# Kernel tuning notes

Measured on AMD Instinct MI355X. Metric: run time of the kernel, lower is better.

The kernel has to match this reference:

```python
import math
import jax, jax.numpy as jnp
import numpy as np

B, D, E, R, TOP_K = 16384, 2048, 64, 128, 2
TAU = 1.0
CAP_FACTOR = 1.25
TOP_C = min(E, max(4, 2 * TOP_K))  # GatingNetwork default top_c


def setup_inputs() -> dict:
    key = jax.random.key(0)
    ks = jax.random.split(key, 7)
    x = jax.random.normal(ks[0], (B, D), dtype=jnp.float32)
    # shared_encoder: nn.Linear(d, d) -> weight [out, in], bias [out]
    We = jax.random.normal(ks[1], (D, D), dtype=jnp.float32) / np.sqrt(D)
    be = jnp.zeros((D,), dtype=jnp.float32)
    # gating: nn.Linear(d, E, bias=False) -> weight [E, d]
    Wg = jax.random.normal(ks[2], (E, D), dtype=jnp.float32) / np.sqrt(D)
    # LowRankExpert per expert: U [r, d], V [d, r], gamma scalar (init 1.0)
    U = jax.random.normal(ks[3], (E, R, D), dtype=jnp.float32) / np.sqrt(D)
    V = jax.random.normal(ks[4], (E, D, R), dtype=jnp.float32) / np.sqrt(R)
    gamma = jnp.ones((E,), dtype=jnp.float32)
    return {"x": x, "We": We, "be": be, "Wg": Wg, "U": U, "V": V, "gamma": gamma}


def reference(x, We, be, Wg, U, V, gamma):
    # shared encoder
    enc = x @ We.T + be  # [B, D]

    # ---- gating: top-C candidates then top-K routing ----
    logits = (enc @ Wg.T) / TAU  # [B, E]
    topc_vals, topc_idx = jax.lax.top_k(logits, TOP_C)          # [B, C]
    topk_vals, pos_in_c = jax.lax.top_k(topc_vals, TOP_K)       # [B, K]
    topk_idx = jnp.take_along_axis(topc_idx, pos_in_c, axis=1)  # [B, K]
    # masked stable softmax over the K selected logits (with 1e-12 eps as in source)
    m = jnp.max(topk_vals, axis=-1, keepdims=True)
    ex = jnp.exp(topk_vals - m)
    w = ex / (jnp.sum(ex, axis=-1, keepdims=True) + 1e-12)      # [B, K]

    # ---- flatten assignments ----
    N = B * TOP_K
    tok = jnp.repeat(jnp.arange(B), TOP_K)   # [N]
    eid = topk_idx.reshape(-1)               # [N]
    wf = w.reshape(-1)                       # [N]
    wmask = wf > 1e-12

    # ---- capacity-based dispatch (sort/group equivalent, fixed shapes) ----
    cap = int(math.ceil(CAP_FACTOR * N / E))  # expert capacity
    onehot = ((eid[:, None] == jnp.arange(E)[None, :]) & wmask[:, None]).astype(jnp.int32)  # [N, E]
    pos = jnp.cumsum(onehot, axis=0) - onehot                      # position within expert
    pos_of = jnp.take_along_axis(pos, eid[:, None], axis=1)[:, 0]  # [N]
    valid = wmask & (pos_of < cap)
    slot = jnp.where(valid, pos_of, cap)  # overflow -> dummy slot (never occurs at this cap)

    # gather tokens to per-expert buffers [E, cap+1, D]
    xbuf = jnp.zeros((E, cap + 1, D), dtype=enc.dtype).at[eid, slot].set(enc[tok])

    # batched low-rank experts: delta = gamma * V @ silu(U @ x)
    h = jax.nn.silu(jnp.einsum('ecd,erd->ecr', xbuf, U))
    delta = jnp.einsum('ecr,edr->ecd', h, V) * gamma[:, None, None]  # [E, cap+1, D]

    # scatter-combine: y = enc + sum_k w_k * delta_k (residual handled since sum w = 1)
    dflat = delta[eid, slot]  # [N, D]
    y = enc.at[tok].add(jnp.where(valid, wf, 0.0)[:, None] * dflat)
    return y
```

## Files before the change

### kernel.cpp

```cpp
#include <hip/hip_runtime.h>
#include <math.h>

#define NTOK 16384
#define DDIM 2048
#define NEXP 64
#define RRANK 128
#define CAP 640

typedef __attribute__((ext_vector_type(8))) short bf16x8;
typedef __attribute__((ext_vector_type(4))) float f32x4;
typedef __attribute__((address_space(1))) const unsigned int gu32_t;
typedef __attribute__((address_space(3))) unsigned int lu32_t;

__device__ __forceinline__ void gload16(const void* g, void* l) {
  __builtin_amdgcn_global_load_lds((gu32_t*)g, (lu32_t*)l, 16, 0, 0);
}

__device__ __forceinline__ float silu_f(float v) {
  return v / (1.f + expf(-v));
}

__device__ __forceinline__ unsigned short f2bf(float f) {
  unsigned int u = __float_as_uint(f);
  unsigned int r = (u + 0x7fffu + ((u >> 16) & 1u)) >> 16;
  return (unsigned short)r;
}

__device__ __forceinline__ float bf2f(unsigned short u) {
  return __uint_as_float(((unsigned int)u) << 16);
}

__device__ __forceinline__ int swz256(int d) {
  return d ^ (((d >> 8) & 7) << 4);
}

__global__ __launch_bounds__(256) void cvt_all_kernel(
    const float* __restrict__ x, const float* __restrict__ We,
    const float* __restrict__ U, const float* __restrict__ V,
    unsigned short* __restrict__ xb, unsigned short* __restrict__ Web,
    unsigned short* __restrict__ Ub, unsigned short* __restrict__ Vb)
{
  const int S0 = NTOK * DDIM / 4;
  const int S1 = DDIM * DDIM / 4;
  const int S2 = NEXP * RRANK * DDIM / 4;
  const int total = S0 + S1 + 2 * S2;
  int i = blockIdx.x * 256 + threadIdx.x;
  const int stride = gridDim.x * 256;
  for (; i < total; i += stride) {
    const float* in; unsigned short* out; int j;
    if (i < S0) { in = x; out = xb; j = i; }
    else if (i < S0 + S1) { in = We; out = Web; j = i - S0; }
    else if (i < S0 + S1 + S2) { in = U; out = Ub; j = i - S0 - S1; }
    else { in = V; out = Vb; j = i - S0 - S1 - S2; }
    const float4 v = ((const float4*)in)[j];
    ushort4 o;
    o.x = f2bf(v.x); o.y = f2bf(v.y); o.z = f2bf(v.z); o.w = f2bf(v.w);
    ((ushort4*)out)[j] = o;
  }
}

__global__ __launch_bounds__(256) void enc_mfma4(
    const unsigned short* __restrict__ xb, const unsigned short* __restrict__ Web,
    const float* __restrict__ be, unsigned short* __restrict__ encbf)
{
  __shared__ unsigned short At[128 * 64];
  __shared__ unsigned short Bt[128 * 64];
  const int tid = threadIdx.x;
  const int lane = tid & 63, wid = tid >> 6;
  const int wr = wid >> 1, wc = wid & 1;
  const int fr = lane & 15, fq = lane >> 4;
  const int bid = blockIdx.x;
  const int wg = (bid & 7) * 256 + (bid >> 3);
  const int n0 = (wg & 15) * 128, m0 = (wg >> 4) * 128;

  const unsigned short* asrc[4];
  const unsigned short* bsrc[4];
  char* adst[4];
  char* bdst[4];
#pragma unroll
  for (int is = 0; is < 4; ++is) {
    const int doff = is * 4096 + tid * 16;
    const int r = doff >> 7;
    const int cs = ((doff >> 4) & 7) ^ (r & 7);
    asrc[is] = xb + (size_t)(m0 + r) * DDIM + cs * 8;
    bsrc[is] = Web + (size_t)(n0 + r) * DDIM + cs * 8;
    adst[is] = (char*)At + doff;
    bdst[is] = (char*)Bt + doff;
  }

  f32x4 acc[4][4];
#pragma unroll
  for (int m = 0; m < 4; ++m)
#pragma unroll
    for (int n = 0; n < 4; ++n) acc[m][n] = (f32x4){0.f, 0.f, 0.f, 0.f};

  for (int kb = 0; kb < DDIM; kb += 64) {
    __syncthreads();
#pragma unroll
    for (int is = 0; is < 4; ++is) {
      gload16(asrc[is] + kb, adst[is]);
      gload16(bsrc[is] + kb, bdst[is]);
    }
    __syncthreads();
#pragma unroll
    for (int kk = 0; kk < 2; ++kk) {
      bf16x8 af[4], bfv[4];
#pragma unroll
      for (int m = 0; m < 4; ++m) {
        const int row = wr * 64 + m * 16 + fr;
        af[m] = *(const bf16x8*)((const char*)At +
                 row * 128 + (((kk * 4 + fq) ^ (row & 7)) << 4));
      }
#pragma unroll
      for (int n = 0; n < 4; ++n) {
        const int row = wc * 64 + n * 16 + fr;
        bfv[n] = *(const bf16x8*)((const char*)Bt +
                  row * 128 + (((kk * 4 + fq) ^ (row & 7)) << 4));
      }
#pragma unroll
      for (int m = 0; m < 4; ++m)
#pragma unroll
        for (int n = 0; n < 4; ++n)
          acc[m][n] = __builtin_amdgcn_mfma_f32_16x16x32_bf16(af[m], bfv[n], acc[m][n], 0, 0, 0);
    }
  }

  float bias[4];
#pragma unroll
  for (int n = 0; n < 4; ++n) bias[n] = be[n0 + wc * 64 + n * 16 + fr];
#pragma unroll
  for (int m = 0; m < 4; ++m) {
#pragma unroll
    for (int j = 0; j < 4; ++j) {
      const int row = m0 + wr * 64 + m * 16 + fq * 4 + j;
      unsigned short* ob = encbf + (size_t)row * DDIM + n0 + wc * 64 + fr;
#pragma unroll
      for (int n = 0; n < 4; ++n)
        ob[n * 16] = f2bf(acc[m][n][j] + bias[n]);
    }
  }
}

__global__ __launch_bounds__(256) void gmat_part_kernel(
    const float* __restrict__ We, const float* __restrict__ Wg,
    double* __restrict__ Gpart)
{
  __shared__ float As[64][68];
  __shared__ float Bs[64][68];
  const int tid = threadIdx.x;
  const int d0 = blockIdx.x * 64;
  const int oc = blockIdx.y;
  const int tx = tid & 15, ty = tid >> 4;
  const int row = tid >> 2, p = (tid & 3) * 16;

  double acc[4][4];
#pragma unroll
  for (int j = 0; j < 4; ++j)
#pragma unroll
    for (int i = 0; i < 4; ++i) acc[j][i] = 0.0;

  for (int o0 = oc * 256; o0 < oc * 256 + 256; o0 += 64) {
    float4 wv[4], gv[4];
#pragma unroll
    for (int q = 0; q < 4; ++q) {
      wv[q] = *(const float4*)(We + (size_t)(o0 + row) * DDIM + d0 + p + q * 4);
      gv[q] = *(const float4*)(Wg + (size_t)row * DDIM + o0 + p + q * 4);
    }
    __syncthreads();
#pragma unroll
    for (int q = 0; q < 4; ++q) {
      const int c = p + q * 4;
      As[row][c + 0] = wv[q].x; As[row][c + 1] = wv[q].y;
      As[row][c + 2] = wv[q].z; As[row][c + 3] = wv[q].w;
      Bs[c + 0][row] = gv[q].x; Bs[c + 1][row] = gv[q].y;
      Bs[c + 2][row] = gv[q].z; Bs[c + 3][row] = gv[q].w;
    }
    __syncthreads();
#pragma unroll 8
    for (int oo = 0; oo < 64; ++oo) {
      double a[4], b[4];
#pragma unroll
      for (int j = 0; j < 4; ++j) a[j] = (double)As[oo][ty * 4 + j];
#pragma unroll
      for (int i = 0; i < 4; ++i) b[i] = (double)Bs[oo][tx * 4 + i];
#pragma unroll
      for (int j = 0; j < 4; ++j)
#pragma unroll
        for (int i = 0; i < 4; ++i)
          acc[j][i] = fma(a[j], b[i], acc[j][i]);
    }
    __syncthreads();
  }
#pragma unroll
  for (int j = 0; j < 4; ++j)
#pragma unroll
    for (int i = 0; i < 4; ++i) {
      const int d = d0 + ty * 4 + j, e = tx * 4 + i;
      Gpart[(size_t)oc * (DDIM * NEXP) + (size_t)e * DDIM + d] = acc[j][i];
    }
}

__global__ __launch_bounds__(256) void greduce_kernel(
    const double* __restrict__ Gpart, double* __restrict__ Gt,
    unsigned short* __restrict__ Gbf)
{
  const int idx = blockIdx.x * 256 + threadIdx.x;
  double s = 0.0;
#pragma unroll
  for (int oc = 0; oc < 8; ++oc)
    s += Gpart[(size_t)oc * (DDIM * NEXP) + idx];
  Gt[idx] = s;
  Gbf[idx] = f2bf((float)s);
}

__global__ __launch_bounds__(256) void bias_c_kernel(
    const float* __restrict__ be, const float* __restrict__ Wg,
    double* __restrict__ c64)
{
  const int e = blockIdx.x;
  const int tid = threadIdx.x;
  double s = 0.0;
  for (int o = tid; o < DDIM; o += 256)
    s += (double)be[o] * (double)Wg[(size_t)e * DDIM + o];
  __shared__ double red[256];
  red[tid] = s;
  __syncthreads();
  for (int st = 128; st > 0; st >>= 1) {
    if (tid < st) red[tid] += red[tid + st];
    __syncthreads();
  }
  if (tid == 0) c64[e] = red[0];
}

__global__ __launch_bounds__(256) void logits_topc_kernel(
    const unsigned short* __restrict__ xb, const unsigned short* __restrict__ Gbf,
    const double* __restrict__ c64, int* __restrict__ cand8)
{
  __shared__ unsigned short At[128 * 32];
  __shared__ unsigned short Bt[64 * 32];
  __shared__ float Ls[128][64];
  const int tid = threadIdx.x;
  const int lane = tid & 63, wid = tid >> 6;
  const int fr = lane & 15, fq = lane >> 4;
  const int t0 = blockIdx.x * 128;

  const int doff0 = wid * 1024 + lane * 16;
  const int doff1 = doff0 + 4096;
  const unsigned short* as0 = xb + (size_t)(t0 + (doff0 >> 6)) * DDIM + ((doff0 & 63) >> 1);
  const unsigned short* as1 = xb + (size_t)(t0 + (doff1 >> 6)) * DDIM + ((doff1 & 63) >> 1);
  const unsigned short* bs0 = Gbf + (size_t)(doff0 >> 6) * DDIM + ((doff0 & 63) >> 1);
  char* ad0 = (char*)At + doff0; char* ad1 = (char*)At + doff1;
  char* bd0 = (char*)Bt + doff0;

  f32x4 acc[2][4];
#pragma unroll
  for (int m = 0; m < 2; ++m)
#pragma unroll
    for (int n = 0; n < 4; ++n) acc[m][n] = (f32x4){0.f, 0.f, 0.f, 0.f};

  for (int kb = 0; kb < DDIM; kb += 32) {
    __syncthreads();
    gload16(as0 + kb, ad0);
    gload16(as1 + kb, ad1);
    gload16(bs0 + kb, bd0);
    __syncthreads();
    bf16x8 af[2], bfr[4];
#pragma unroll
    for (int m = 0; m < 2; ++m)
      af[m] = *(const bf16x8*)&At[(wid * 32 + m * 16 + fr) * 32 + fq * 8];
#pragma unroll
    for (int n = 0; n < 4; ++n)
      bfr[n] = *(const bf16x8*)&Bt[(n * 16 + fr) * 32 + fq * 8];
#pragma unroll
    for (int m = 0; m < 2; ++m)
#pragma unroll
      for (int n = 0; n < 4; ++n)
        acc[m][n] = __builtin_amdgcn_mfma_f32_16x16x32_bf16(af[m], bfr[n], acc[m][n], 0, 0, 0);
  }

#pragma unroll
  for (int m = 0; m < 2; ++m)
#pragma unroll
    for (int j = 0; j < 4; ++j) {
      const int row = wid * 32 + m * 16 + fq * 4 + j;
#pragma unroll
      for (int n = 0; n < 4; ++n)
        Ls[row][n * 16 + fr] = acc[m][n][j];
    }
  __syncthreads();

  if (tid < 128) {
    float v8[8];
    int i8[8];
#pragma unroll
    for (int c = 0; c < 8; ++c) { v8[c] = -INFINITY; i8[c] = 0; }
    for (int e = 0; e < NEXP; ++e) {
      const float v = Ls[tid][e] + (float)c64[e];
      if (v > v8[7]) {
        int p = 7;
        while (p > 0 && v > v8[p - 1]) { v8[p] = v8[p - 1]; i8[p] = i8[p - 1]; --p; }
        v8[p] = v; i8[p] = e;
      }
    }
    int* cp = cand8 + (size_t)(t0 + tid) * 8;
#pragma unroll
    for (int c = 0; c < 8; ++c) cp[c] = i8[c];
  }
}

__global__ __launch_bounds__(256) void refine_kernel(
    const float* __restrict__ x, const double* __restrict__ Gt,
    const double* __restrict__ c64, const int* __restrict__ cand8,
    int* __restrict__ topk, float* __restrict__ wkf)
{
  const int t = blockIdx.x;
  const int tid = threadIdx.x;
  const int lane = tid & 63, w = tid >> 6;
  __shared__ float xs[DDIM];
  __shared__ double red[8][4];

  ((float4*)xs)[tid] = ((const float4*)(x + (size_t)t * DDIM))[tid];
  ((float4*)xs)[tid + 256] = ((const float4*)(x + (size_t)t * DDIM))[tid + 256];
  __syncthreads();

  int myc[8];
#pragma unroll
  for (int c = 0; c < 8; ++c) myc[c] = cand8[(size_t)t * 8 + c];

#pragma unroll
  for (int c = 0; c < 8; ++c) {
    const double* g = Gt + (size_t)myc[c] * DDIM;
    double s = 0.0;
#pragma unroll
    for (int q = 0; q < 8; ++q) {
      const int d = q * 256 + tid;
      s += (double)xs[d] * g[d];
    }
#pragma unroll
    for (int off = 32; off > 0; off >>= 1) s += __shfl_down(s, off);
    if (lane == 0) red[c][w] = s;
  }
  __syncthreads();

  if (tid == 0) {
    double v1 = -1e300, v2 = -1e300;
    int i1 = 0, i2 = 0;
#pragma unroll
    for (int c = 0; c < 8; ++c) {
      const double v = red[c][0] + red[c][1] + red[c][2] + red[c][3] + c64[myc[c]];
      if (v > v1) { v2 = v1; i2 = i1; v1 = v; i1 = myc[c]; }
      else if (v > v2) { v2 = v; i2 = myc[c]; }
    }
    const double e2 = exp(v2 - v1);
    const double s = 1.0 + e2 + 1e-12;
    topk[2 * t] = i1; topk[2 * t + 1] = i2;
    wkf[2 * t] = (float)(1.0 / s);
    wkf[2 * t + 1] = (float)(e2 / s);
  }
}

__global__ __launch_bounds__(256) void route_kernel(
    const int* __restrict__ topk, const float* __restrict__ wkf,
    int* __restrict__ slots , int* __restrict__ counts_eff,
    int* __restrict__ val )
{
  const int e = blockIdx.x;
  const int tid = threadIdx.x;
  const int lane = tid & 63, wave = tid >> 6;
  const int base0 = wave * 8192;
  __shared__ int wcnt[4];

  int cnt = 0;
  for (int c = 0; c < 8192; c += 64) {
    const int a = base0 + c + lane;
    const bool match = (topk[a] == e) && (wkf[a] > 1e-12f);
    cnt += (int)__popcll(__ballot(match));
  }
  if (lane == 0) wcnt[wave] = cnt;
  __syncthreads();

  int run = 0;
  for (int w = 0; w < 4; ++w)
    if (w < wave) run += wcnt[w];
  const int total = wcnt[0] + wcnt[1] + wcnt[2] + wcnt[3];

  for (int c = 0; c < 8192; c += 64) {
    const int a = base0 + c + lane;
    const bool match = (topk[a] == e) && (wkf[a] > 1e-12f);
    const unsigned long long bal = __ballot(match);
    const int rank = run + (int)__popcll(bal & ((1ull << lane) - 1ull));
    if (match && rank < CAP) {
      slots[e * CAP + rank] = a;
      val[a] = 1;
    }
    run += (int)__popcll(bal);
  }
  if (tid == 0) counts_eff[e] = (total < CAP) ? total : CAP;
}

__global__ __launch_bounds__(256) void expert_fused(
    const unsigned short* __restrict__ encbf, const unsigned short* __restrict__ Ub,
    const unsigned short* __restrict__ Vb, const float* __restrict__ gamma,
    const int* __restrict__ counts_eff, const int* __restrict__ slots,
    const float* __restrict__ wkf, unsigned short* __restrict__ Dbuf)
{
  const int lin = blockIdx.x;
  const int wg = (lin & 7) * 80 + (lin >> 3);
  const int e = wg / 10;
  const int t0 = (wg % 10) * 64;
  const int cnt = counts_eff[e];
  if (t0 >= cnt) return;

  __shared__ int aid[64];
  __shared__ int toks[64];
  __shared__ float wts[64];
  __shared__ unsigned short Ht[64 * 128];
  __shared__ char U2[32768];

  const int tid = threadIdx.x;
  const int lane = tid & 63, wid = tid >> 6;
  const int wr = wid >> 1, wc = wid & 1;
  const int fr = lane & 15, fq = lane >> 4;

  if (tid < 64) {
    const int i = t0 + tid;
    if (i < cnt) {
      const int a = slots[e * CAP + i];
      aid[tid] = a;
      toks[tid] = a >> 1;
      wts[tid] = wkf[a] * gamma[e];
    } else {
      aid[tid] = -1;
      toks[tid] = slots[e * CAP] >> 1;
      wts[tid] = 0.f;
    }
  }
  __syncthreads();

  unsigned short* At = (unsigned short*)U2;
  unsigned short* Bt = (unsigned short*)(U2 + 8192);
  const unsigned short* Ue = Ub + (size_t)e * RRANK * DDIM;

  size_t aoff[2]; char* adst[2];
#pragma unroll
  for (int is = 0; is < 2; ++is) {
    const int doff = is * 4096 + tid * 16;
    const int r = doff >> 7;
    const int cs = ((doff >> 4) & 7) ^ (r & 7);
    aoff[is] = (size_t)toks[r] * DDIM + cs * 8;
    adst[is] = (char*)At + doff;
  }
  const unsigned short* bsrc[4]; char* bdst[4];
#pragma unroll
  for (int is = 0; is < 4; ++is) {
    const int doff = is * 4096 + tid * 16;
    const int r = doff >> 7;
    const int cs = ((doff >> 4) & 7) ^ (r & 7);
    bsrc[is] = Ue + (size_t)r * DDIM + cs * 8;
    bdst[is] = (char*)Bt + doff;
  }

  f32x4 hacc[2][4];
#pragma unroll
  for (int m = 0; m < 2; ++m)
#pragma unroll
    for (int n = 0; n < 4; ++n) hacc[m][n] = (f32x4){0.f, 0.f, 0.f, 0.f};

  for (int kb = 0; kb < DDIM; kb += 64) {
    __syncthreads();
    gload16(encbf + aoff[0] + kb, adst[0]);
    gload16(encbf + aoff[1] + kb, adst[1]);
#pragma unroll
    for (int is = 0; is < 4; ++is)
      gload16(bsrc[is] + kb, bdst[is]);
    __syncthreads();
#pragma unroll
    for (int kk = 0; kk < 2; ++kk) {
      bf16x8 af[2], bfv[4];
#pragma unroll
      for (int m = 0; m < 2; ++m) {
        const int row = wr * 32 + m * 16 + fr;
        af[m] = *(const bf16x8*)((const char*)At +
                 row * 128 + (((kk * 4 + fq) ^ (row & 7)) << 4));
      }
#pragma unroll
      for (int n = 0; n < 4; ++n) {
        const int row = wc * 64 + n * 16 + fr;
        bfv[n] = *(const bf16x8*)((const char*)Bt +
                  row * 128 + (((kk * 4 + fq) ^ (row & 7)) << 4));
      }
#pragma unroll
      for (int m = 0; m < 2; ++m)
#pragma unroll
        for (int n = 0; n < 4; ++n)
          hacc[m][n] = __builtin_amdgcn_mfma_f32_16x16x32_bf16(af[m], bfv[n], hacc[m][n], 0, 0, 0);
    }
  }

  __syncthreads();
#pragma unroll
  for (int m = 0; m < 2; ++m) {
#pragma unroll
    for (int j = 0; j < 4; ++j) {
      const int row = wr * 32 + m * 16 + fq * 4 + j;
#pragma unroll
      for (int n = 0; n < 4; ++n) {
        const int col = wc * 64 + n * 16 + fr;
        const int b = (row * 256 + col * 2) ^ ((row & 7) << 4);
        *(unsigned short*)((char*)Ht + b) = f2bf(silu_f(hacc[m][n][j]));
      }
    }
  }
  __syncthreads();

  unsigned short* Vt = (unsigned short*)U2;
  const unsigned short* Ve = Vb + (size_t)e * DDIM * RRANK;
  const int hd = tid * 16;

  bf16x8 paf[2][4];
  float wv[2][4];
  int av[2][4];
#pragma unroll
  for (int m = 0; m < 2; ++m) {
    const int row = wr * 32 + m * 16 + fr;
#pragma unroll
    for (int kk = 0; kk < 4; ++kk) {
      const int b = (row * 256 + kk * 64 + fq * 16) ^ ((row & 7) << 4);
      paf[m][kk] = *(const bf16x8*)((const char*)Ht + b);
    }
#pragma unroll
    for (int j = 0; j < 4; ++j) {
      const int tl = wr * 32 + m * 16 + fq * 4 + j;
      wv[m][j] = wts[tl];
      av[m][j] = aid[tl];
    }
  }

  for (int nb = 0; nb < 16; ++nb) {
    __syncthreads();
    const unsigned short* vsrc = Ve + (size_t)nb * 128 * RRANK;
#pragma unroll
    for (int is = 0; is < 8; ++is) {
      const int d = is * 4096 + hd;
      gload16(vsrc + (swz256(d) >> 1), (char*)Vt + d);
    }
    __syncthreads();

    f32x4 acc[2][4];
#pragma unroll
    for (int m = 0; m < 2; ++m)
#pragma unroll
      for (int n = 0; n < 4; ++n) acc[m][n] = (f32x4){0.f, 0.f, 0.f, 0.f};

#pragma unroll
    for (int n = 0; n < 4; ++n) {
      const int drow = wc * 64 + n * 16 + fr;
#pragma unroll
      for (int kk = 0; kk < 4; ++kk) {
        const int b = (drow * 256 + kk * 64 + fq * 16) ^ ((drow & 7) << 4);
        const bf16x8 bfr = *(const bf16x8*)((const char*)Vt + b);
#pragma unroll
        for (int m = 0; m < 2; ++m)
          acc[m][n] = __builtin_amdgcn_mfma_f32_16x16x32_bf16(paf[m][kk], bfr, acc[m][n], 0, 0, 0);
      }
    }

#pragma unroll
    for (int m = 0; m < 2; ++m) {
#pragma unroll
      for (int j = 0; j < 4; ++j) {
        if (av[m][j] >= 0) {
          const float w = wv[m][j];
          unsigned short* dp = Dbuf + (size_t)av[m][j] * DDIM + nb * 128 + wc * 64 + fr;
#pragma unroll
          for (int n = 0; n < 4; ++n)
            dp[n * 16] = f2bf(acc[m][n][j] * w);
        }
      }
    }
  }
}

__global__ __launch_bounds__(256) void combine_kernel(
    const unsigned short* __restrict__ encbf, const unsigned short* __restrict__ Dbuf,
    const int* __restrict__ val, float* __restrict__ y)
{
  const int t = blockIdx.x;
  const int tid = threadIdx.x;
  const int c0 = tid * 8;
  float* yp = y + (size_t)t * DDIM + c0;
  const int v0 = val[2 * t], v1 = val[2 * t + 1];

  const ushort4 e0 = *(const ushort4*)(encbf + (size_t)t * DDIM + c0);
  const ushort4 e1 = *(const ushort4*)(encbf + (size_t)t * DDIM + c0 + 4);
  float o[8] = {bf2f(e0.x), bf2f(e0.y), bf2f(e0.z), bf2f(e0.w),
                bf2f(e1.x), bf2f(e1.y), bf2f(e1.z), bf2f(e1.w)};

  if (v0) {
    const ushort4 d0 = *(const ushort4*)(Dbuf + (size_t)(2 * t) * DDIM + c0);
    const ushort4 d1 = *(const ushort4*)(Dbuf + (size_t)(2 * t) * DDIM + c0 + 4);
    o[0] += bf2f(d0.x); o[1] += bf2f(d0.y); o[2] += bf2f(d0.z); o[3] += bf2f(d0.w);
    o[4] += bf2f(d1.x); o[5] += bf2f(d1.y); o[6] += bf2f(d1.z); o[7] += bf2f(d1.w);
  }
  if (v1) {
    const ushort4 d0 = *(const ushort4*)(Dbuf + (size_t)(2 * t + 1) * DDIM + c0);
    const ushort4 d1 = *(const ushort4*)(Dbuf + (size_t)(2 * t + 1) * DDIM + c0 + 4);
    o[0] += bf2f(d0.x); o[1] += bf2f(d0.y); o[2] += bf2f(d0.z); o[3] += bf2f(d0.w);
    o[4] += bf2f(d1.x); o[5] += bf2f(d1.y); o[6] += bf2f(d1.z); o[7] += bf2f(d1.w);
  }
  *(float4*)(yp) = (float4){o[0], o[1], o[2], o[3]};
  *(float4*)(yp + 4) = (float4){o[4], o[5], o[6], o[7]};
}

extern "C" void kernel_launch(void* const* d_in, const int* in_sizes, int n_in,
                              void* d_out, int out_size, void* d_ws, size_t ws_size,
                              hipStream_t stream)
{
  const float* x     = (const float*)d_in[0];
  const float* We    = (const float*)d_in[1];
  const float* be    = (const float*)d_in[2];
  const float* Wg    = (const float*)d_in[3];
  const float* U     = (const float*)d_in[4];
  const float* V     = (const float*)d_in[5];
  const float* gamma = (const float*)d_in[6];
  float* y = (float*)d_out;

  char* ws = (char*)d_ws;
  int*            topk       = (int*)(ws + 0);
  float*          wkf        = (float*)(ws + 131072);
  int*            counts_eff = (int*)(ws + 262144);
  double*         c64        = (double*)(ws + 262400);
  int*            cand8      = (int*)(ws + 262912);
  double*         Gt         = (double*)(ws + 787200);
  unsigned short* G_bf       = (unsigned short*)(ws + 1835776);
  int*            slots      = (int*)(ws + 2097920);
  int*            val        = (int*)(ws + 2261760);
  unsigned short* Dbuf       = (unsigned short*)(ws + 2392832);
  unsigned short* x_bf       = (unsigned short*)(ws + 2392832);
  unsigned short* We_bf      = (unsigned short*)(ws + 69501696);
  double*         Gpart      = (double*)(ws + 77890304);
  unsigned short* U_bf       = (unsigned short*)(ws + 136610560);
  unsigned short* V_bf       = (unsigned short*)(ws + 170164992);
  unsigned short* enc_bf     = (unsigned short*)(ws + 203719424);

  hipMemsetAsync(val, 0, 131072, stream);

  cvt_all_kernel<<<dim3(2048), 256, 0, stream>>>(x, We, U, V, x_bf, We_bf, U_bf, V_bf);

  gmat_part_kernel<<<dim3(32, 8), 256, 0, stream>>>(We, Wg, Gpart);
  greduce_kernel<<<dim3(512), 256, 0, stream>>>(Gpart, Gt, G_bf);
  bias_c_kernel<<<dim3(64), 256, 0, stream>>>(be, Wg, c64);
  logits_topc_kernel<<<dim3(128), 256, 0, stream>>>(x_bf, G_bf, c64, cand8);
  refine_kernel<<<dim3(NTOK), 256, 0, stream>>>(x, Gt, c64, cand8, topk, wkf);
  route_kernel<<<dim3(64), 256, 0, stream>>>(topk, wkf, slots, counts_eff, val);

  enc_mfma4<<<dim3(2048), 256, 0, stream>>>(x_bf, We_bf, be, enc_bf);
  expert_fused<<<dim3(640), 256, 0, stream>>>(enc_bf, U_bf, V_bf, gamma, counts_eff, slots, wkf, Dbuf);
  combine_kernel<<<dim3(NTOK), 256, 0, stream>>>(enc_bf, Dbuf, val, y);
}
```

Measured before the change: 731.3 us.

## Double-buffer encoder GEMM with 256x256 tiles and async LDS prefetch

Rewrites the shared encoder bf16 GEMM to use 256x256 block tiles with 512 threads and a double-buffered LDS pipeline. The next k-slab is prefetched via global_load_lds while MFMAs run on the current one, using explicit vmcnt waits and s_setprio around the MFMA bursts. This aims to hide global memory latency and raise data reuse per tile. In exchange it uses 128 KB of LDS and more accumulator registers, which limits occupancy to one block per CU.

```diff
diff --git a/kernel.cpp b/kernel.cpp
--- a/kernel.cpp
+++ b/kernel.cpp
@@ -59,80 +59,110 @@
   }
 }
 
-__global__ __launch_bounds__(256) void enc_mfma4(
+__global__ __launch_bounds__(512, 2) void enc_mfma5(
     const unsigned short* __restrict__ xb, const unsigned short* __restrict__ Web,
     const float* __restrict__ be, unsigned short* __restrict__ encbf)
 {
-  __shared__ unsigned short At[128 * 64];
-  __shared__ unsigned short Bt[128 * 64];
+  __shared__ unsigned short LDS[65536];
   const int tid = threadIdx.x;
   const int lane = tid & 63, wid = tid >> 6;
-  const int wr = wid >> 1, wc = wid & 1;
+  const int wr = wid >> 2, wc = wid & 3;
   const int fr = lane & 15, fq = lane >> 4;
   const int bid = blockIdx.x;
-  const int wg = (bid & 7) * 256 + (bid >> 3);
-  const int n0 = (wg & 15) * 128, m0 = (wg >> 4) * 128;
-
-  const unsigned short* asrc[4];
-  const unsigned short* bsrc[4];
-  char* adst[4];
-  char* bdst[4];
+  const int wg = (bid & 7) * 64 + (bid >> 3);
+  const int n0 = (wg & 7) * 256, m0 = (wg >> 3) * 256;
+
+  const unsigned short* asb[4];
+  const unsigned short* bsb[4];
+  int d4[4];
 #pragma unroll
   for (int is = 0; is < 4; ++is) {
-    const int doff = is * 4096 + tid * 16;
+    const int doff = is * 8192 + tid * 16;
     const int r = doff >> 7;
     const int cs = ((doff >> 4) & 7) ^ (r & 7);
-    asrc[is] = xb + (size_t)(m0 + r) * DDIM + cs * 8;
-    bsrc[is] = Web + (size_t)(n0 + r) * DDIM + cs * 8;
-    adst[is] = (char*)At + doff;
-    bdst[is] = (char*)Bt + doff;
-  }
-
-  f32x4 acc[4][4];
-#pragma unroll
-  for (int m = 0; m < 4; ++m)
+    asb[is] = xb + (size_t)(m0 + r) * DDIM + cs * 8;
+    bsb[is] = Web + (size_t)(n0 + r) * DDIM + cs * 8;
+    d4[is] = doff;
+  }
+
+  auto STAGE = [&](int buf, int kb) {
+#pragma unroll
+    for (int is = 0; is < 4; ++is) {
+      gload16(asb[is] + kb, (char*)(LDS + buf * 16384) + d4[is]);
+      gload16(bsb[is] + kb, (char*)(LDS + 32768 + buf * 16384) + d4[is]);
+    }
+  };
+
+  f32x4 acc[8][4];
+#pragma unroll
+  for (int m = 0; m < 8; ++m)
 #pragma unroll
     for (int n = 0; n < 4; ++n) acc[m][n] = (f32x4){0.f, 0.f, 0.f, 0.f};
 
-  for (int kb = 0; kb < DDIM; kb += 64) {
-    __syncthreads();
-#pragma unroll
-    for (int is = 0; is < 4; ++is) {
-      gload16(asrc[is] + kb, adst[is]);
-      gload16(bsrc[is] + kb, bdst[is]);
-    }
-    __syncthreads();
-#pragma unroll
-    for (int kk = 0; kk < 2; ++kk) {
-      bf16x8 af[4], bfv[4];
+  STAGE(0, 0);
+  STAGE(1, 64);
+  asm volatile("s_waitcnt vmcnt(8)" ::: "memory");
+  __builtin_amdgcn_s_barrier();
+  asm volatile("" ::: "memory");
+
+#pragma unroll 1
+  for (int t = 0; t < 32; ++t) {
+    const int cur = t & 1;
+    const unsigned short* Ab = LDS + cur * 16384;
+    const unsigned short* Bb = LDS + 32768 + cur * 16384;
+
+    bf16x8 bfv[4][2];
+#pragma unroll
+    for (int n = 0; n < 4; ++n) {
+      const int row = wc * 64 + n * 16 + fr;
+#pragma unroll
+      for (int kk = 0; kk < 2; ++kk)
+        bfv[n][kk] = *(const bf16x8*)((const char*)Bb +
+                      row * 128 + (((kk * 4 + fq) ^ (row & 7)) << 4));
+    }
+#pragma unroll
+    for (int mh = 0; mh < 2; ++mh) {
+      bf16x8 af[4][2];
 #pragma unroll
       for (int m = 0; m < 4; ++m) {
-        const int row = wr * 64 + m * 16 + fr;
-        af[m] = *(const bf16x8*)((const char*)At +
-                 row * 128 + (((kk * 4 + fq) ^ (row & 7)) << 4));
+        const int row = wr * 128 + (mh * 4 + m) * 16 + fr;
+#pragma unroll
+        for (int kk = 0; kk < 2; ++kk)
+          af[m][kk] = *(const bf16x8*)((const char*)Ab +
+                       row * 128 + (((kk * 4 + fq) ^ (row & 7)) << 4));
       }
-#pragma unroll
-      for (int n = 0; n < 4; ++n) {
-        const int row = wc * 64 + n * 16 + fr;
-        bfv[n] = *(const bf16x8*)((const char*)Bt +
-                  row * 128 + (((kk * 4 + fq) ^ (row & 7)) << 4));
-      }
+      __builtin_amdgcn_s_setprio(1);
 #pragma unroll
       for (int m = 0; m < 4; ++m)
 #pragma unroll
         for (int n = 0; n < 4; ++n)
-          acc[m][n] = __builtin_amdgcn_mfma_f32_16x16x32_bf16(af[m], bfv[n], acc[m][n], 0, 0, 0);
-    }
+#pragma unroll
+          for (int kk = 0; kk < 2; ++kk)
+            acc[mh * 4 + m][n] = __builtin_amdgcn_mfma_f32_16x16x32_bf16(
+                af[m][kk], bfv[n][kk], acc[mh * 4 + m][n], 0, 0, 0);
+      __builtin_amdgcn_s_setprio(0);
+    }
+
+    asm volatile("" ::: "memory");
+    __builtin_amdgcn_s_barrier();
+    if (t < 30) {
+      STAGE(cur, (t + 2) * 64);
+      asm volatile("s_waitcnt vmcnt(8)" ::: "memory");
+    } else {
+      asm volatile("s_waitcnt vmcnt(0)" ::: "memory");
+    }
+    __builtin_amdgcn_s_barrier();
+    asm volatile("" ::: "memory");
   }
 
   float bias[4];
 #pragma unroll
   for (int n = 0; n < 4; ++n) bias[n] = be[n0 + wc * 64 + n * 16 + fr];
 #pragma unroll
-  for (int m = 0; m < 4; ++m) {
+  for (int m = 0; m < 8; ++m) {
 #pragma unroll
     for (int j = 0; j < 4; ++j) {
-      const int row = m0 + wr * 64 + m * 16 + fq * 4 + j;
+      const int row = m0 + wr * 128 + m * 16 + fq * 4 + j;
       unsigned short* ob = encbf + (size_t)row * DDIM + n0 + wc * 64 + fr;
 #pragma unroll
       for (int n = 0; n < 4; ++n)
@@ -654,7 +684,7 @@
   refine_kernel<<<dim3(NTOK), 256, 0, stream>>>(x, Gt, c64, cand8, topk, wkf);
   route_kernel<<<dim3(64), 256, 0, stream>>>(topk, wkf, slots, counts_eff, val);
 
-  enc_mfma4<<<dim3(2048), 256, 0, stream>>>(x_bf, We_bf, be, enc_bf);
+  enc_mfma5<<<dim3(512), 512, 0, stream>>>(x_bf, We_bf, be, enc_bf);
   expert_fused<<<dim3(640), 256, 0, stream>>>(enc_bf, U_bf, V_bf, gamma, counts_eff, slots, wkf, Dbuf);
   combine_kernel<<<dim3(NTOK), 256, 0, stream>>>(enc_bf, Dbuf, val, y);
 }
```

New measurement: 702.5 us. 1.04x faster.
